# Kernel tuning notes

Hardware: AMD Instinct MI355X
Metric: run time of the kernel (lower is better)

Reference implementation:

```python
import jax, jax.numpy as jnp
import numpy as np

B, S, F = 8, 1024, 512
E, H = 64, 16  # embed_dim per head, n_heads (match init_kwargs)


def setup_inputs() -> dict:
    key = jax.random.key(0)
    k1, k2, k3, k4, k5, k6 = jax.random.split(key, 6)
    inputs1 = jax.random.normal(k1, (B, S, F), dtype=jnp.float32)
    inputs2 = jax.random.normal(k2, (B, S, F), dtype=jnp.float32)
    W_kv = jax.random.normal(k3, (F, E * H * 2), dtype=jnp.float32) * 0.02
    b_kv = jax.random.normal(k4, (E * H * 2,), dtype=jnp.float32) * 0.02
    W_q = jax.random.normal(k5, (F, E * H), dtype=jnp.float32) * 0.02
    b_q = jax.random.normal(k6, (E * H,), dtype=jnp.float32) * 0.02
    return {"inputs1": inputs1, "inputs2": inputs2,
            "W_kv": W_kv, "b_kv": b_kv, "W_q": W_q, "b_q": b_q}


def reference(inputs1, inputs2, W_kv, b_kv, W_q, b_q):
    scaling = 1.0 / jnp.sqrt(jnp.float32(E))
    # KV path: Dense then reshape (B,S,E,H,2) -> transpose to (B,2,H,S,E)
    kv = inputs1 @ W_kv + b_kv                      # (B,S,E*H*2), layout d-major
    kv = kv.reshape(B, S, E, H, 2)
    kv = jnp.transpose(kv, (0, 4, 3, 1, 2))        # (B,2,H,S,E)
    k = kv[:, 0]                                   # (B,H,S,E)
    v = kv[:, 1]                                   # (B,H,S,E)
    # Q path: Dense then reshape (B,S,E,H) -> (B,H,S,E)
    q = (inputs2 @ W_q + b_q).reshape(B, S, E, H)
    q = jnp.transpose(q, (0, 3, 1, 2))             # (B,H,S,E)
    # Attention: softmax FIRST, then scale (non-standard, faithful to source)
    qk = jnp.einsum('bhqe,bhke->bhqk', q, k)       # (B,H,S,S)
    attn = jax.nn.softmax(qk, axis=-1) * scaling
    out = jnp.einsum('bhqk,bhke->bhqe', attn, v)   # (B,H,S,E)
    out = jnp.transpose(out, (0, 2, 1, 3))         # (B,S,H,E)
    return out.reshape(B, S, E * H)
```

## Files before the change

### kernel.cpp

```cpp
#include <hip/hip_runtime.h>
#include <hip/hip_bf16.h>
#include <math.h>

#define NB 8
#define NS 1024
#define NF 512
#define NE 64
#define NH 16

typedef __attribute__((ext_vector_type(8))) short short8;
typedef __attribute__((ext_vector_type(4))) float floatx4;

__device__ inline unsigned short f2bf(float f) {
  union { float f; unsigned int u; } c; c.f = f;
  unsigned int u = c.u;
  u += 0x7FFFu + ((u >> 16) & 1u);
  return (unsigned short)(u >> 16);
}

__device__ inline unsigned int cvt_pk_bf16(float a, float b) {
  unsigned int r;
  asm("v_cvt_pk_bf16_f32 %0, %1, %2" : "=v"(r) : "v"(a), "v"(b));
  return r;
}

__device__ inline float fexp2(float x) {
#if __has_builtin(__builtin_amdgcn_exp2f)
  return __builtin_amdgcn_exp2f(x);
#else
  return exp2f(x);
#endif
}

__device__ inline void gl_lds16(const void* g, void* l) {
  __builtin_amdgcn_global_load_lds(
      (const __attribute__((address_space(1))) unsigned int*)g,
      (__attribute__((address_space(3))) unsigned int*)l, 16, 0, 0);
}

__global__ __launch_bounds__(256) void perm_w_dual(
    const float* __restrict__ Wkv, const float* __restrict__ Wq,
    unsigned short* __restrict__ Wtkv, unsigned short* __restrict__ Wtq)
{
  __shared__ float T[64][65];
  const int t = threadIdx.x;
  const int k0 = blockIdx.y * 64;
  const int bx = blockIdx.x;
  const float* W;
  unsigned short* Wt;
  int N, n0, logg;
  if (bx < 32) { W = Wkv; Wt = Wtkv; N = 2048; n0 = bx * 64; logg = 5; }
  else         { W = Wq;  Wt = Wtq;  N = 1024; n0 = (bx - 32) * 64; logg = 4; }

  #pragma unroll
  for (int p = 0; p < 4; ++p) {
    int i = (t >> 4) + p * 16, j = (t & 15) * 4;
    float4 v = *(const float4*)(W + (size_t)(k0 + i) * N + n0 + j);
    T[i][j] = v.x; T[i][j + 1] = v.y; T[i][j + 2] = v.z; T[i][j + 3] = v.w;
  }
  __syncthreads();
  #pragma unroll
  for (int p = 0; p < 2; ++p) {
    int c = p * 256 + t;
    int jn = c >> 3, kc = (c & 7) * 8;
    int n = n0 + jn;
    int g = n & ((1 << logg) - 1), e = n >> logg;
    unsigned short v[8];
    #pragma unroll
    for (int j = 0; j < 8; ++j) v[j] = f2bf(T[kc + j][jn]);
    *(uint4*)(Wt + (size_t)(g * 64 + e) * NF + k0 + kc) = *(uint4*)v;
  }
}

union GemmLds {
  struct { unsigned short A[2][128 * 32]; unsigned short B[2][128 * 32]; } ab;
  unsigned short C[128 * 136];
  struct { unsigned short K[128][72]; unsigned short V[64][136]; } kv;
};

template <int MODE>
__device__ __forceinline__ void gemm_body(
    const float* __restrict__ A32, const unsigned short* __restrict__ Wt,
    const float* __restrict__ bias, unsigned short* __restrict__ out0,
    unsigned short* __restrict__ out1, GemmLds& u, int bid)
{
  const int t = threadIdx.x;
  const int w = t >> 6, l = t & 63;
  const int quad = l >> 4, l16 = l & 15;
  const int NX = (MODE == 0) ? 16 : 8;
  const int nwg = NX * 64;
  const int swz = (bid & 7) * (nwg >> 3) + (bid >> 3);
  const int n0 = (swz % NX) * 128, m0 = (swz / NX) * 128;
  const int wm = (w >> 1) * 64, wn = (w & 1) * 64;

  floatx4 acc[4][4];
  #pragma unroll
  for (int mi = 0; mi < 4; ++mi)
    #pragma unroll
    for (int nj = 0; nj < 4; ++nj) acc[mi][nj] = (floatx4){0.f, 0.f, 0.f, 0.f};

  const int cswz = (l & 3) ^ ((l >> 3) & 3);
  const int rswz = (l16 >> 1) & 3;

  const float* Ag = A32 + (size_t)(m0 + w * 16 + (l >> 2)) * NF + (l & 3) * 8;
  const unsigned short* Bg = Wt + (size_t)(n0 + w * 16 + (l >> 2)) * NF + cswz * 8;

  auto stageA = [&](int buf, int k0) {
    #pragma unroll
    for (int hf = 0; hf < 2; ++hf) {
      const float* src = Ag + (size_t)hf * 64 * NF + k0;
      float4 fa = *(const float4*)src;
      float4 fb = *(const float4*)(src + 4);
      uint4 pk;
      pk.x = cvt_pk_bf16(fa.x, fa.y); pk.y = cvt_pk_bf16(fa.z, fa.w);
      pk.z = cvt_pk_bf16(fb.x, fb.y); pk.w = cvt_pk_bf16(fb.z, fb.w);
      *(uint4*)&u.ab.A[buf][(hf * 64 + w * 16 + (l >> 2)) * 32 + cswz * 8] = pk;
    }
  };

  stageA(0, 0);
  gl_lds16(Bg,           &u.ab.B[0][(w * 16) * 32]);
  gl_lds16(Bg + 64 * NF, &u.ab.B[0][(64 + w * 16) * 32]);

  for (int kt = 0; kt < 16; ++kt) {
    __syncthreads();
    const int cur = kt & 1;
    if (kt < 15) {
      const int k0 = (kt + 1) * 32;
      stageA(cur ^ 1, k0);
      gl_lds16(Bg + k0,           &u.ab.B[cur ^ 1][(w * 16) * 32]);
      gl_lds16(Bg + 64 * NF + k0, &u.ab.B[cur ^ 1][(64 + w * 16) * 32]);
    }
    short8 af[4], bf[4];
    #pragma unroll
    for (int mi = 0; mi < 4; ++mi)
      af[mi] = *(const short8*)
          &u.ab.A[cur][(wm + mi * 16 + l16) * 32 + (quad ^ rswz) * 8];
    #pragma unroll
    for (int nj = 0; nj < 4; ++nj)
      bf[nj] = *(const short8*)
          &u.ab.B[cur][(wn + nj * 16 + l16) * 32 + (quad ^ rswz) * 8];
    #pragma unroll
    for (int mi = 0; mi < 4; ++mi)
      #pragma unroll
      for (int nj = 0; nj < 4; ++nj)
        acc[mi][nj] = __builtin_amdgcn_mfma_f32_16x16x32_bf16(
            af[mi], bf[nj], acc[mi][nj], 0, 0, 0);
  }

  float bv[4];
  #pragma unroll
  for (int nj = 0; nj < 4; ++nj) {
    int np = n0 + wn + nj * 16 + l16;
    int n = (MODE == 0) ? ((np & 63) * 32 + (np >> 6)) : ((np & 63) * 16 + (np >> 6));
    bv[nj] = bias[n];
  }
  __syncthreads();

  if (MODE == 0) {
    if (wn == 0) {
      #pragma unroll
      for (int mi = 0; mi < 4; ++mi)
        #pragma unroll
        for (int nj = 0; nj < 4; ++nj)
          #pragma unroll
          for (int r = 0; r < 4; ++r)
            u.kv.K[wm + mi * 16 + quad * 4 + r][nj * 16 + l16] =
                f2bf(acc[mi][nj][r] + bv[nj]);
    } else {
      #pragma unroll
      for (int mi = 0; mi < 4; ++mi)
        #pragma unroll
        for (int nj = 0; nj < 4; ++nj)
          #pragma unroll
          for (int r = 0; r < 4; ++r)
            u.kv.V[nj * 16 + l16][wm + mi * 16 + quad * 4 + r] =
                f2bf(acc[mi][nj][r] + bv[nj]);
    }
  } else {
    const float LOG2E = 1.44269504088896f;
    #pragma unroll
    for (int mi = 0; mi < 4; ++mi)
      #pragma unroll
      for (int nj = 0; nj < 4; ++nj)
        #pragma unroll
        for (int r = 0; r < 4; ++r)
          u.C[(wm + mi * 16 + quad * 4 + r) * 136 + wn + nj * 16 + l16] =
              f2bf((acc[mi][nj][r] + bv[nj]) * LOG2E);
  }
  __syncthreads();

  if (MODE == 0) {
    const int h = n0 >> 7, btile = m0 >> 10, s0 = m0 & 1023;
    #pragma unroll
    for (int p = 0; p < 4; ++p) {
      int c = p * 256 + t;
      int m = c >> 3, ec = c & 7;
      uint4 v = *(const uint4*)&u.kv.K[m][ec * 8];
      *(uint4*)(out0 + (((size_t)btile * NH + h) * NS + s0 + m) * NE + ec * 8) = v;
    }
    #pragma unroll
    for (int p = 0; p < 4; ++p) {
      int c = p * 256 + t;
      int e = c >> 4, mc = c & 15;
      uint4 v = *(const uint4*)&u.kv.V[e][mc * 8];
      *(uint4*)(out1 + (((size_t)btile * NH + h) * NE + e) * NS + s0 + mc * 8) = v;
    }
  } else {
    #pragma unroll
    for (int p = 0; p < 8; ++p) {
      int c = p * 256 + t;
      int m = c >> 4, col8 = (c & 15) * 8;
      uint4 v = *(const uint4*)&u.C[m * 136 + col8];
      int mg = m0 + m, b = mg >> 10, s = mg & 1023;
      int h = (n0 >> 6) + (col8 >> 6), e0 = col8 & 63;
      *(uint4*)(out0 + (((size_t)b * NH + h) * NS + s) * NE + e0) = v;
    }
  }
}

__global__ __launch_bounds__(256) void gemm_fused(
    const float* __restrict__ in1, const float* __restrict__ in2,
    const unsigned short* __restrict__ Wtkv, const unsigned short* __restrict__ Wtq,
    const float* __restrict__ b_kv, const float* __restrict__ b_q,
    unsigned short* __restrict__ Kb, unsigned short* __restrict__ Vtb,
    unsigned short* __restrict__ Qb)
{
  __shared__ GemmLds u;
  const int bid = blockIdx.x;
  if (bid < 1024) gemm_body<0>(in1, Wtkv, b_kv, Kb, Vtb, u, bid);
  else            gemm_body<1>(in2, Wtq,  b_q,  Qb, nullptr, u, bid - 1024);
}

__global__ __launch_bounds__(256, 2) void attn_kernel(
    const unsigned short* __restrict__ Q, const unsigned short* __restrict__ K,
    const unsigned short* __restrict__ Vt, float* __restrict__ out)
{
  __shared__ unsigned short Ks[2][64][64];
  __shared__ unsigned short Vs[2][64][64];

  const int t = threadIdx.x;
  const int w = t >> 6, lane = t & 63;
  const int quad = lane >> 4, l16 = lane & 15;
  const int n = blockIdx.x;
  const int qt = n >> 7;
  const int g = n & 127;
  const int h = g & 15, b = g >> 4;
  const size_t bh = ((size_t)b * NH + h) * NS * NE;
  const int q0 = qt * 256 + w * 64;

  short8 aq[4][2];
  #pragma unroll
  for (int rb = 0; rb < 4; ++rb) {
    const unsigned short* qrow = Q + bh + (size_t)(q0 + rb * 16 + l16) * NE;
    aq[rb][0] = *(const short8*)(qrow + quad * 8);
    aq[rb][1] = *(const short8*)(qrow + 32 + quad * 8);
  }

  const int sr = t >> 3, sc8 = t & 7;
  const int xs = (sc8 ^ (sr & 7)) * 8;
  const int xq = (quad ^ (l16 & 7)) * 8;
  const unsigned short* Kg = K + bh;
  const unsigned short* Vg = Vt + bh;

  {
    *(uint4*)&Ks[0][sr][xs]      = *(const uint4*)(Kg + (size_t)sr * NE + sc8 * 8);
    *(uint4*)&Ks[0][32 + sr][xs] = *(const uint4*)(Kg + (size_t)(32 + sr) * NE + sc8 * 8);
    *(uint4*)&Vs[0][sr][xs]      = *(const uint4*)(Vg + (size_t)sr * NS + sc8 * 8);
    *(uint4*)&Vs[0][32 + sr][xs] = *(const uint4*)(Vg + (size_t)(32 + sr) * NS + sc8 * 8);
  }

  float lsum[4] = {0.f, 0.f, 0.f, 0.f};
  floatx4 O[4][4];
  #pragma unroll
  for (int rb = 0; rb < 4; ++rb)
    #pragma unroll
    for (int j = 0; j < 4; ++j) O[rb][j] = (floatx4){0.f, 0.f, 0.f, 0.f};

  for (int kt = 0; kt < NS / 64; ++kt) {
    __syncthreads();
    const int bi = kt & 1;

    uint4 kn0, kn1, vn0, vn1;
    if (kt < 15) {
      const unsigned short* kg = Kg + (size_t)(kt + 1) * 64 * NE;
      kn0 = *(const uint4*)(kg + (size_t)sr * NE + sc8 * 8);
      kn1 = *(const uint4*)(kg + (size_t)(32 + sr) * NE + sc8 * 8);
      const unsigned short* vg = Vg + (kt + 1) * 64;
      vn0 = *(const uint4*)(vg + (size_t)sr * NS + sc8 * 8);
      vn1 = *(const uint4*)(vg + (size_t)(32 + sr) * NS + sc8 * 8);
    }

    short8 kf0[4], kf1[4];
    #pragma unroll
    for (int kb = 0; kb < 4; ++kb) {
      kf0[kb] = *(const short8*)&Ks[bi][kb * 16 + l16][xq];
      kf1[kb] = *(const short8*)&Ks[bi][kb * 16 + l16][xq ^ 32];
    }

    short8 paf[4][2];
    #pragma unroll
    for (int rb = 0; rb < 4; ++rb) {
      floatx4 st[4];
      __builtin_amdgcn_s_setprio(1);
      #pragma unroll
      for (int kb = 0; kb < 4; ++kb) {
        floatx4 z = (floatx4){0.f, 0.f, 0.f, 0.f};
        z = __builtin_amdgcn_mfma_f32_16x16x32_bf16(kf0[kb], aq[rb][0], z, 0, 0, 0);
        st[kb] = __builtin_amdgcn_mfma_f32_16x16x32_bf16(kf1[kb], aq[rb][1], z, 0, 0, 0);
      }
      __builtin_amdgcn_s_setprio(0);
      unsigned int c[4][2];
      #pragma unroll
      for (int kb = 0; kb < 4; ++kb) {
        float p0 = fexp2(st[kb][0]), p1 = fexp2(st[kb][1]);
        float p2 = fexp2(st[kb][2]), p3 = fexp2(st[kb][3]);
        lsum[rb] += (p0 + p1) + (p2 + p3);
        c[kb][0] = cvt_pk_bf16(p0, p1);
        c[kb][1] = cvt_pk_bf16(p2, p3);
      }
      #pragma unroll
      for (int m = 0; m < 2; ++m) {
        union { unsigned int wd[4]; short8 v; } pu;
        #pragma unroll
        for (int j = 0; j < 2; ++j) {
          unsigned int a = c[2 * m][j], bb = c[2 * m + 1][j];
          asm("v_permlane32_swap_b32 %0, %1" : "+v"(a), "+v"(bb));
          asm("v_permlane16_swap_b32 %0, %1" : "+v"(a), "+v"(bb));
          pu.wd[j]     = a;
          pu.wd[2 + j] = bb;
        }
        paf[rb][m] = pu.v;
      }
    }

    short8 vf0[4], vf1[4];
    #pragma unroll
    for (int eb = 0; eb < 4; ++eb) {
      vf0[eb] = *(const short8*)&Vs[bi][eb * 16 + l16][xq];
      vf1[eb] = *(const short8*)&Vs[bi][eb * 16 + l16][xq ^ 32];
    }
    __builtin_amdgcn_s_setprio(1);
    #pragma unroll
    for (int rb = 0; rb < 4; ++rb) {
      #pragma unroll
      for (int eb = 0; eb < 4; ++eb) {
        O[rb][eb] = __builtin_amdgcn_mfma_f32_16x16x32_bf16(paf[rb][0], vf0[eb], O[rb][eb], 0, 0, 0);
        O[rb][eb] = __builtin_amdgcn_mfma_f32_16x16x32_bf16(paf[rb][1], vf1[eb], O[rb][eb], 0, 0, 0);
      }
    }
    __builtin_amdgcn_s_setprio(0);

    if (kt < 15) {
      const int bn = bi ^ 1;
      *(uint4*)&Ks[bn][sr][xs]      = kn0;
      *(uint4*)&Ks[bn][32 + sr][xs] = kn1;
      *(uint4*)&Vs[bn][sr][xs]      = vn0;
      *(uint4*)&Vs[bn][32 + sr][xs] = vn1;
    }
  }

  const float scaling = 0.125f;
  #pragma unroll
  for (int rb = 0; rb < 4; ++rb) {
    float lv = lsum[rb];
    lv += __shfl_xor(lv, 16);
    lv += __shfl_xor(lv, 32);
    #pragma unroll
    for (int r = 0; r < 4; ++r) {
      float inv = scaling / __shfl(lv, quad * 4 + r);
      int s = q0 + rb * 16 + quad * 4 + r;
      float* orow = out + ((size_t)b * NS + s) * (NE * NH) + h * NE;
      orow[l16]      = O[rb][0][r] * inv;
      orow[16 + l16] = O[rb][1][r] * inv;
      orow[32 + l16] = O[rb][2][r] * inv;
      orow[48 + l16] = O[rb][3][r] * inv;
    }
  }
}

extern "C" void kernel_launch(void* const* d_in, const int* in_sizes, int n_in,
                              void* d_out, int out_size, void* d_ws, size_t ws_size,
                              hipStream_t stream) {
  const float* inputs1 = (const float*)d_in[0];
  const float* inputs2 = (const float*)d_in[1];
  const float* W_kv    = (const float*)d_in[2];
  const float* b_kv    = (const float*)d_in[3];
  const float* W_q     = (const float*)d_in[4];
  const float* b_q     = (const float*)d_in[5];
  float* out = (float*)d_out;

  const size_t plane = (size_t)NB * NH * NS * NE;
  unsigned short* Qb   = (unsigned short*)d_ws;
  unsigned short* Kb   = Qb + plane;
  unsigned short* Vtb  = Kb + plane;
  unsigned short* Wtkv = Vtb + plane;
  unsigned short* Wtq  = Wtkv + (size_t)2048 * NF;

  dim3 blk(256);
  perm_w_dual<<<dim3(48, NF / 64), blk, 0, stream>>>(W_kv, W_q, Wtkv, Wtq);
  gemm_fused<<<dim3(1536), blk, 0, stream>>>(
      inputs1, inputs2, Wtkv, Wtq, b_kv, b_q, Kb, Vtb, Qb);
  attn_kernel<<<dim3(512), blk, 0, stream>>>(Qb, Kb, Vtb, out);
}
```

Measured before the change: 94.39 us.

## Write V-transpose directly from registers and shrink GEMM epilogue LDS

In the KV projection epilogue, the V half now converts accumulators to packed bf16 and stores them straight to the transposed global V layout, so it no longer stages through LDS. Only K goes through LDS. The Q staging buffer loses its padding, which shrinks the LDS union, and launch bounds now request 5 blocks per CU to raise occupancy. The costs are narrower 8-byte scattered global stores for V, possible LDS bank conflicts on the unpadded C buffer, and register pressure from the occupancy hint.

New measurement: 103.1 us. +9.3%, slower.

```diff
diff --git a/kernel.cpp b/kernel.cpp
--- a/kernel.cpp
+++ b/kernel.cpp
@@ -74,8 +74,8 @@
 
 union GemmLds {
   struct { unsigned short A[2][128 * 32]; unsigned short B[2][128 * 32]; } ab;
-  unsigned short C[128 * 136];
-  struct { unsigned short K[128][72]; unsigned short V[64][136]; } kv;
+  unsigned short K[128 * 72];
+  unsigned short C[128 * 128];
 };
 
 template <int MODE>
@@ -158,6 +158,7 @@
   __syncthreads();
 
   if (MODE == 0) {
+    const int h = n0 >> 7, btile = m0 >> 10, s0 = m0 & 1023;
     if (wn == 0) {
       #pragma unroll
       for (int mi = 0; mi < 4; ++mi)
@@ -165,17 +166,29 @@
         for (int nj = 0; nj < 4; ++nj)
           #pragma unroll
           for (int r = 0; r < 4; ++r)
-            u.kv.K[wm + mi * 16 + quad * 4 + r][nj * 16 + l16] =
+            u.K[(wm + mi * 16 + quad * 4 + r) * 72 + nj * 16 + l16] =
                 f2bf(acc[mi][nj][r] + bv[nj]);
     } else {
       #pragma unroll
       for (int mi = 0; mi < 4; ++mi)
         #pragma unroll
-        for (int nj = 0; nj < 4; ++nj)
-          #pragma unroll
-          for (int r = 0; r < 4; ++r)
-            u.kv.V[nj * 16 + l16][wm + mi * 16 + quad * 4 + r] =
-                f2bf(acc[mi][nj][r] + bv[nj]);
+        for (int nj = 0; nj < 4; ++nj) {
+          uint2 pk;
+          pk.x = cvt_pk_bf16(acc[mi][nj][0] + bv[nj], acc[mi][nj][1] + bv[nj]);
+          pk.y = cvt_pk_bf16(acc[mi][nj][2] + bv[nj], acc[mi][nj][3] + bv[nj]);
+          int e = nj * 16 + l16;
+          size_t off = (((size_t)btile * NH + h) * NE + e) * NS +
+                       s0 + wm + mi * 16 + quad * 4;
+          *(uint2*)(out1 + off) = pk;
+        }
+    }
+    __syncthreads();
+    #pragma unroll
+    for (int p = 0; p < 4; ++p) {
+      int c = p * 256 + t;
+      int m = c >> 3, ec = c & 7;
+      uint4 v = *(const uint4*)&u.K[m * 72 + ec * 8];
+      *(uint4*)(out0 + (((size_t)btile * NH + h) * NS + s0 + m) * NE + ec * 8) = v;
     }
   } else {
     const float LOG2E = 1.44269504088896f;
@@ -185,33 +198,14 @@
       for (int nj = 0; nj < 4; ++nj)
         #pragma unroll
         for (int r = 0; r < 4; ++r)
-          u.C[(wm + mi * 16 + quad * 4 + r) * 136 + wn + nj * 16 + l16] =
+          u.C[(wm + mi * 16 + quad * 4 + r) * 128 + wn + nj * 16 + l16] =
               f2bf((acc[mi][nj][r] + bv[nj]) * LOG2E);
-  }
-  __syncthreads();
-
-  if (MODE == 0) {
-    const int h = n0 >> 7, btile = m0 >> 10, s0 = m0 & 1023;
-    #pragma unroll
-    for (int p = 0; p < 4; ++p) {
-      int c = p * 256 + t;
-      int m = c >> 3, ec = c & 7;
-      uint4 v = *(const uint4*)&u.kv.K[m][ec * 8];
-      *(uint4*)(out0 + (((size_t)btile * NH + h) * NS + s0 + m) * NE + ec * 8) = v;
-    }
-    #pragma unroll
-    for (int p = 0; p < 4; ++p) {
-      int c = p * 256 + t;
-      int e = c >> 4, mc = c & 15;
-      uint4 v = *(const uint4*)&u.kv.V[e][mc * 8];
-      *(uint4*)(out1 + (((size_t)btile * NH + h) * NE + e) * NS + s0 + mc * 8) = v;
-    }
-  } else {
+    __syncthreads();
     #pragma unroll
     for (int p = 0; p < 8; ++p) {
       int c = p * 256 + t;
       int m = c >> 4, col8 = (c & 15) * 8;
-      uint4 v = *(const uint4*)&u.C[m * 136 + col8];
+      uint4 v = *(const uint4*)&u.C[m * 128 + col8];
       int mg = m0 + m, b = mg >> 10, s = mg & 1023;
       int h = (n0 >> 6) + (col8 >> 6), e0 = col8 & 63;
       *(uint4*)(out0 + (((size_t)b * NH + h) * NS + s) * NE + e0) = v;
@@ -219,7 +213,7 @@
   }
 }
 
-__global__ __launch_bounds__(256) void gemm_fused(
+__global__ __launch_bounds__(256, 5) void gemm_fused(
     const float* __restrict__ in1, const float* __restrict__ in2,
     const unsigned short* __restrict__ Wtkv, const unsigned short* __restrict__ Wtq,
     const float* __restrict__ b_kv, const float* __restrict__ b_q,
```
